# Performance work log

Hardware: AMD Instinct MI355X
Metric: run time of the kernel (lower is better)

## Reference

```python
import jax, jax.numpy as jnp
import numpy as np

C_IN = 256
C_RED = max(4, C_IN // 4)  # 64


def setup_inputs() -> dict:
    key = jax.random.key(0)
    k1, k2, k3, k4, k5 = jax.random.split(key, 5)
    B, C, H, W = 4, C_IN, 64, 64
    x = jax.random.normal(k1, (B, C, H, W), dtype=jnp.float32)
    # 1x1 convs (no bias) are just channel matmuls: weight shape (out_ch, in_ch)
    s_in = 1.0 / np.sqrt(C)
    s_red = 1.0 / np.sqrt(C_RED)
    Wq = jax.random.normal(k2, (C_RED, C), dtype=jnp.float32) * s_in
    Wk = jax.random.normal(k3, (C_RED, C), dtype=jnp.float32) * s_in
    Wv = jax.random.normal(k4, (C_RED, C), dtype=jnp.float32) * s_in
    Wp = jax.random.normal(k5, (C, C_RED), dtype=jnp.float32) * s_red
    return {"x": x, "Wq": Wq, "Wk": Wk, "Wv": Wv, "Wp": Wp}


def reference(x, Wq, Wk, Wv, Wp):
    B, C, H, W = x.shape
    N = H * W
    xf = x.reshape(B, C, N)                       # (B, C, N)
    q = jnp.einsum('rc,bcn->bnr', Wq, xf)         # (B, N, c_red)
    k = jnp.einsum('rc,bcn->brn', Wk, xf)         # (B, c_red, N)
    v = jnp.einsum('rc,bcn->bnr', Wv, xf)         # (B, N, c_red)
    scale = 1.0 / jnp.sqrt(jnp.float32(k.shape[1]))
    attn = jnp.einsum('bnr,brm->bnm', q, k) * scale   # (B, N, N)
    attn = jax.nn.softmax(attn, axis=-1)
    out = jnp.einsum('bnm,bmr->brn', attn, v)     # (B, c_red, N)
    out = jnp.einsum('cr,brn->bcn', Wp, out)      # (B, C, N)
    return out.reshape(B, C, H, W) + x
```

## Files before the change

### kernel.cpp

```cpp
#include <hip/hip_runtime.h>
#include <hip/hip_bf16.h>

#define CIN 256
#define CRED 64
#define NB 4
#define NN 4096

typedef float v4f __attribute__((ext_vector_type(4)));
typedef short v8s __attribute__((ext_vector_type(8)));
typedef unsigned short u16;
typedef u16 u16x4 __attribute__((ext_vector_type(4)));
typedef u16 u16x8 __attribute__((ext_vector_type(8)));
typedef unsigned int u32;

#define LOG2E 1.4426950408889634f

__device__ __forceinline__ u16 f2bf(float f) {
    union { float f; u32 u; } v; v.f = f;
    u32 r = (v.u + 0x7FFFu + ((v.u >> 16) & 1u)) >> 16;
    return (u16)r;
}
__device__ __forceinline__ float bf2f(u16 s) {
    union { u32 u; float f; } v; v.u = ((u32)s) << 16;
    return v.f;
}
__device__ __forceinline__ v4f mfma16(v8s a, v8s b, v4f c) {
    return __builtin_amdgcn_mfma_f32_16x16x32_bf16(a, b, c, 0, 0, 0);
}
__device__ __forceinline__ float fexp2(float x) {
#if __has_builtin(__builtin_amdgcn_exp2f)
    return __builtin_amdgcn_exp2f(x);
#else
    return exp2f(x);
#endif
}

__global__ __launch_bounds__(256) void k_wconv(const float* __restrict__ Wq,
                                               const float* __restrict__ Wk,
                                               const float* __restrict__ Wv,
                                               const float* __restrict__ Wp,
                                               u16* __restrict__ Wb,
                                               u16* __restrict__ WpB) {
    int t = threadIdx.x;
    if (blockIdx.x < 48) {
        int idx = (blockIdx.x * 256 + t) * 4;
        int row = idx >> 8;
        int mat = row >> 6, r = row & 63, col = idx & 255;
        const float* src = (mat == 0) ? Wq : (mat == 1) ? Wk : Wv;
        float4 v = *(const float4*)&src[r * 256 + col];
        float s = (mat == 0) ? (0.125f * LOG2E) : 1.0f;
        u16x4 o;
        o[0] = f2bf(v.x * s); o[1] = f2bf(v.y * s);
        o[2] = f2bf(v.z * s); o[3] = f2bf(v.w * s);
        *(u16x4*)&Wb[idx] = o;
    } else {
        int idx = ((blockIdx.x - 48) * 256 + t) * 4;
        float4 v = *(const float4*)&Wp[idx];
        u16x4 o;
        o[0] = f2bf(v.x); o[1] = f2bf(v.y);
        o[2] = f2bf(v.z); o[3] = f2bf(v.w);
        *(u16x4*)&WpB[idx] = o;
    }
}

#define XP 264
__global__ __launch_bounds__(256, 2) void k_qkvm(const float* __restrict__ x,
                                                 const u16* __restrict__ Wb,
                                                 u16* __restrict__ Q, u16* __restrict__ K,
                                                 u16* __restrict__ V) {
    __shared__ u16 xT[32 * XP];
    __shared__ u16 Vt[4][16 * 20];
    int t = threadIdx.x;
    int wv = t >> 6, lane = t & 63, c15 = lane & 15, quad = lane >> 4;
    int n0g = blockIdx.x * 32;
    int b = n0g >> 12;
    int nb = n0g & 4095;
    const float* xb = x + ((size_t)b << 20) + nb;

#pragma unroll
    for (int i = 0; i < 8; ++i) {
        int f4 = t + i * 256;
        int c = f4 >> 3, j4 = (f4 & 7) * 4;
        float4 v = *(const float4*)&xb[(size_t)c * 4096 + j4];
        xT[(j4 + 0) * XP + c] = f2bf(v.x);
        xT[(j4 + 1) * XP + c] = f2bf(v.y);
        xT[(j4 + 2) * XP + c] = f2bf(v.z);
        xT[(j4 + 3) * XP + c] = f2bf(v.w);
    }
    __syncthreads();

#pragma unroll
    for (int rti = 0; rti < 3; ++rti) {
        int rt = wv * 3 + rti;
        const u16* wrow = Wb + (size_t)(rt * 16 + c15) * 256 + quad * 8;
        v8s Bf[8];
#pragma unroll
        for (int kc = 0; kc < 8; ++kc) Bf[kc] = *(const v8s*)&wrow[kc * 32];
#pragma unroll
        for (int nt = 0; nt < 2; ++nt) {
            v4f acc = {0.f, 0.f, 0.f, 0.f};
            const u16* arow = &xT[(nt * 16 + c15) * XP + quad * 8];
#pragma unroll
            for (int kc = 0; kc < 8; ++kc) {
                v8s Af = *(const v8s*)&arow[kc * 32];
                acc = mfma16(Af, Bf[kc], acc);
            }
            if (rt < 8) {
                u16* base = (rt < 4) ? Q : K;
                u16* dst = base + ((size_t)b << 18)
                         + (size_t)(nb + nt * 16 + quad * 4) * 64
                         + (rt & 3) * 16 + c15;
#pragma unroll
                for (int g = 0; g < 4; ++g) dst[g * 64] = f2bf(acc[g]);
            } else {
                u16* vt = Vt[wv];
#pragma unroll
                for (int g = 0; g < 4; ++g)
                    vt[c15 * 20 + quad * 4 + g] = f2bf(acc[g]);
                int r_loc = lane & 15, ng2 = lane >> 4;
                u16x4 vvv = *(u16x4*)&vt[r_loc * 20 + ng2 * 4];
                size_t va = ((size_t)b * 64 + (rt - 8) * 16 + r_loc) * 4096
                          + nb + nt * 16 + ng2 * 4;
                *(u16x4*)&V[va] = vvv;
            }
        }
    }
}

__global__ __launch_bounds__(256, 4) void k_flash(const u16* __restrict__ Q,
                                                  const u16* __restrict__ K,
                                                  const u16* __restrict__ V,
                                                  u16* __restrict__ OP,
                                                  float* __restrict__ Lb,
                                                  int sh) {
    __shared__ u16 Kl[64][72];
    __shared__ u16 Vl[64][72];
    __shared__ u16 Pl[4][32][72];
    int t = threadIdx.x;
    int p = blockIdx.x & ((1u << sh) - 1);
    int tile = blockIdx.x >> sh;
    int b = tile >> 5;
    int n0 = (tile & 31) * 128;
    int wv = t >> 6;
    int lane = t & 63;
    int c15 = lane & 15;
    int quad = lane >> 4;
    int nw = n0 + wv * 32;
    const u16* Qb = Q + (size_t)b * NN * 64;
    const u16* Kb = K + (size_t)b * NN * 64;
    const u16* Vb = V + (size_t)b * 64 * NN;

    v8s Qa[2][2];
#pragma unroll
    for (int rg = 0; rg < 2; ++rg)
#pragma unroll
        for (int c2 = 0; c2 < 2; ++c2)
            Qa[rg][c2] = *(const v8s*)&Qb[(size_t)(nw + rg * 16 + c15) * 64 + c2 * 32 + quad * 8];

    v4f O[2][4];
    float ls[2][4];
#pragma unroll
    for (int rg = 0; rg < 2; ++rg)
#pragma unroll
        for (int g = 0; g < 4; ++g) {
            ls[rg][g] = 0.f;
#pragma unroll
            for (int cg = 0; cg < 4; ++cg) O[rg][cg][g] = 0.f;
        }

    int mlen = NN >> sh;
    int m0 = p * mlen;
    int iters = mlen >> 6;
    for (int it = 0; it < iters; ++it) {
        int mt = m0 + it * 64;
        int srow = t >> 3, scol = (t & 7) * 8;
#pragma unroll
        for (int pass = 0; pass < 2; ++pass) {
            int rr = srow + pass * 32;
            *(v8s*)&Kl[rr][scol] = *(const v8s*)&Kb[(size_t)(mt + rr) * 64 + scol];
            *(v8s*)&Vl[rr][scol] = *(const v8s*)&Vb[(size_t)rr * NN + mt + scol];
        }
        __syncthreads();

        v4f S[2][4];
#pragma unroll
        for (int rg = 0; rg < 2; ++rg)
#pragma unroll
            for (int s = 0; s < 4; ++s)
#pragma unroll
                for (int g = 0; g < 4; ++g) S[rg][s][g] = 0.f;
#pragma unroll
        for (int s = 0; s < 4; ++s)
#pragma unroll
            for (int c2 = 0; c2 < 2; ++c2) {
                v8s kb = *(const v8s*)&Kl[s * 16 + c15][c2 * 32 + quad * 8];
                S[0][s] = mfma16(Qa[0][c2], kb, S[0][s]);
                S[1][s] = mfma16(Qa[1][c2], kb, S[1][s]);
            }

#pragma unroll
        for (int rg = 0; rg < 2; ++rg)
#pragma unroll
            for (int s = 0; s < 4; ++s)
#pragma unroll
                for (int g = 0; g < 4; ++g) {
                    float e = fexp2(S[rg][s][g]);
                    ls[rg][g] += e;
                    Pl[wv][rg * 16 + quad * 4 + g][s * 16 + c15] = f2bf(e);
                }

        v8s Pa[2][2];
#pragma unroll
        for (int rg = 0; rg < 2; ++rg)
#pragma unroll
            for (int c2 = 0; c2 < 2; ++c2)
                Pa[rg][c2] = *(const v8s*)&Pl[wv][rg * 16 + c15][c2 * 32 + quad * 8];
#pragma unroll
        for (int cg = 0; cg < 4; ++cg)
#pragma unroll
            for (int c2 = 0; c2 < 2; ++c2) {
                v8s vb = *(const v8s*)&Vl[cg * 16 + c15][c2 * 32 + quad * 8];
                O[0][cg] = mfma16(Pa[0][c2], vb, O[0][cg]);
                O[1][cg] = mfma16(Pa[1][c2], vb, O[1][cg]);
            }
        __syncthreads();
    }

    u16* OPp = OP + (size_t)p * (NB * NN * 64) + (size_t)b * NN * 64;
#pragma unroll
    for (int rg = 0; rg < 2; ++rg)
#pragma unroll
        for (int cg = 0; cg < 4; ++cg)
#pragma unroll
            for (int g = 0; g < 4; ++g) {
                int n = nw + rg * 16 + quad * 4 + g;
                OPp[(size_t)n * 64 + cg * 16 + c15] = f2bf(O[rg][cg][g]);
            }
#pragma unroll
    for (int rg = 0; rg < 2; ++rg)
#pragma unroll
        for (int g = 0; g < 4; ++g) {
            float v = ls[rg][g];
#pragma unroll
            for (int off = 1; off <= 8; off <<= 1) v += __shfl_xor(v, off);
            ls[rg][g] = v;
        }
    if (c15 == 0) {
        float* Lp = Lb + (size_t)p * (NB * NN) + (size_t)b * NN;
#pragma unroll
        for (int rg = 0; rg < 2; ++rg)
#pragma unroll
            for (int g = 0; g < 4; ++g) {
                int n = nw + rg * 16 + quad * 4 + g;
                Lp[n] = ls[rg][g];
            }
    }
}

#define OMP 72
__global__ __launch_bounds__(256) void k_proj(const u16* __restrict__ OP,
                                              const float* __restrict__ Lb,
                                              const u16* __restrict__ WpB,
                                              const float* __restrict__ x,
                                              float* __restrict__ out,
                                              int nsp) {
    __shared__ u16 Om[32 * OMP];
    int t = threadIdx.x;
    int b = blockIdx.x >> 7;
    int n0 = (blockIdx.x & 127) * 32;

    {
        int n_l = t >> 3, r0 = (t & 7) * 8;
        size_t nidx = (size_t)b * NN + n0 + n_l;
        float o[8];
#pragma unroll
        for (int j = 0; j < 8; ++j) o[j] = 0.f;
        float l = 0.f;
        for (int p = 0; p < nsp; ++p) {
            u16x8 u = *(const u16x8*)&OP[((size_t)p * (NB * NN) + nidx) * 64 + r0];
#pragma unroll
            for (int j = 0; j < 8; ++j) o[j] += bf2f(u[j]);
            l += Lb[(size_t)p * (NB * NN) + nidx];
        }
        float inv = 1.0f / l;
        u16x8 pk;
#pragma unroll
        for (int j = 0; j < 8; ++j) pk[j] = f2bf(o[j] * inv);
        *(u16x8*)&Om[n_l * OMP + r0] = pk;
    }
    __syncthreads();

    int lane = t & 63, wv = t >> 6, c15 = lane & 15, quad = lane >> 4;
#pragma unroll
    for (int ct0 = 0; ct0 < 4; ++ct0) {
        int ct = wv * 4 + ct0;
        const u16* wrow = WpB + (size_t)(ct * 16 + c15) * 64 + quad * 8;
        v8s A0 = *(const v8s*)&wrow[0];
        v8s A1 = *(const v8s*)&wrow[32];
#pragma unroll
        for (int nt = 0; nt < 2; ++nt) {
            v8s B0 = *(const v8s*)&Om[(nt * 16 + c15) * OMP + quad * 8];
            v8s B1 = *(const v8s*)&Om[(nt * 16 + c15) * OMP + 32 + quad * 8];
            v4f acc = {0.f, 0.f, 0.f, 0.f};
            acc = mfma16(A0, B0, acc);
            acc = mfma16(A1, B1, acc);
            int cb = ct * 16 + quad * 4;
            size_t base = ((size_t)b * 256 + cb) * 4096 + n0 + nt * 16 + c15;
#pragma unroll
            for (int g = 0; g < 4; ++g)
                out[base + (size_t)g * 4096] = acc[g] + x[base + (size_t)g * 4096];
        }
    }
}

extern "C" void kernel_launch(void* const* d_in, const int* in_sizes, int n_in,
                              void* d_out, int out_size, void* d_ws, size_t ws_size,
                              hipStream_t stream) {
    const float* x  = (const float*)d_in[0];
    const float* Wq = (const float*)d_in[1];
    const float* Wk = (const float*)d_in[2];
    const float* Wv = (const float*)d_in[3];
    const float* Wp = (const float*)d_in[4];
    float* out = (float*)d_out;
    char* ws = (char*)d_ws;

    int nsp = (ws_size >= (size_t)24 * 1024 * 1024) ? 8 : 4;
    int sh = (nsp == 8) ? 3 : 2;

    u16* Wb  = (u16*)(ws);
    u16* WpB = (u16*)(ws + 131072);
    u16* Q   = (u16*)(ws + 262144);
    u16* K   = (u16*)(ws + 262144 + 2097152);
    u16* V   = (u16*)(ws + 262144 + 2 * 2097152);
    u16* OP  = (u16*)(ws + 262144 + 3 * 2097152);
    float* Lbuf = (float*)(ws + 262144 + (size_t)(3 + nsp) * 2097152);

    k_wconv<<<64, 256, 0, stream>>>(Wq, Wk, Wv, Wp, Wb, WpB);
    k_qkvm<<<512, 256, 0, stream>>>(x, Wb, Q, K, V);
    k_flash<<<NB * 32 * nsp, 256, 0, stream>>>(Q, K, V, OP, Lbuf, sh);
    k_proj<<<512, 256, 0, stream>>>(OP, Lbuf, WpB, x, out, nsp);
}
```

Before: 127.1 us.

## Load x fragments straight to registers, permute V layout, pack P stores, shrink proj tiles

The QKV projection kernel now builds MFMA A fragments directly from global x with strided scalar loads and packed bf16 conversion, dropping the LDS transpose and its barrier. V is written in a permuted column order so that the flash kernel can store P with packed 4-element writes instead of scalar LDS stores. The flash kernel's P layout changes to match, and the projection kernel uses 16-column tiles with twice as many blocks. Strided uncoalesced global loads of x and scattered V stores may cost more bandwidth than the LDS work they replace.

```diff
diff --git a/kernel.cpp b/kernel.cpp
--- a/kernel.cpp
+++ b/kernel.cpp
@@ -23,6 +23,12 @@
 __device__ __forceinline__ float bf2f(u16 s) {
     union { u32 u; float f; } v; v.u = ((u32)s) << 16;
     return v.f;
+}
+__device__ __forceinline__ u32 pkbf(float a, float b) {
+    float2 f; f.x = a; f.y = b;
+    __hip_bfloat162 h = __float22bfloat162_rn(f);
+    union { __hip_bfloat162 h; u32 u; } c; c.h = h;
+    return c.u;
 }
 __device__ __forceinline__ v4f mfma16(v8s a, v8s b, v4f c) {
     return __builtin_amdgcn_mfma_f32_16x16x32_bf16(a, b, c, 0, 0, 0);
@@ -63,31 +69,32 @@
     }
 }
 
-#define XP 264
-__global__ __launch_bounds__(256, 2) void k_qkvm(const float* __restrict__ x,
-                                                 const u16* __restrict__ Wb,
-                                                 u16* __restrict__ Q, u16* __restrict__ K,
-                                                 u16* __restrict__ V) {
-    __shared__ u16 xT[32 * XP];
-    __shared__ u16 Vt[4][16 * 20];
+__global__ __launch_bounds__(256) void k_qkvm(const float* __restrict__ x,
+                                              const u16* __restrict__ Wb,
+                                              u16* __restrict__ Q, u16* __restrict__ K,
+                                              u16* __restrict__ V) {
     int t = threadIdx.x;
     int wv = t >> 6, lane = t & 63, c15 = lane & 15, quad = lane >> 4;
     int n0g = blockIdx.x * 32;
-    int b = n0g >> 12;
-    int nb = n0g & 4095;
-    const float* xb = x + ((size_t)b << 20) + nb;
-
-#pragma unroll
-    for (int i = 0; i < 8; ++i) {
-        int f4 = t + i * 256;
-        int c = f4 >> 3, j4 = (f4 & 7) * 4;
-        float4 v = *(const float4*)&xb[(size_t)c * 4096 + j4];
-        xT[(j4 + 0) * XP + c] = f2bf(v.x);
-        xT[(j4 + 1) * XP + c] = f2bf(v.y);
-        xT[(j4 + 2) * XP + c] = f2bf(v.z);
-        xT[(j4 + 3) * XP + c] = f2bf(v.w);
-    }
-    __syncthreads();
+    int b = n0g >> 12, nb = n0g & 4095;
+    const float* xb = x + ((size_t)b << 20);
+
+    v8s Af[2][8];
+#pragma unroll
+    for (int nt = 0; nt < 2; ++nt) {
+        const float* px = xb + nb + nt * 16 + c15 + (size_t)quad * 8 * 4096;
+#pragma unroll
+        for (int kc = 0; kc < 8; ++kc) {
+            float f[8];
+#pragma unroll
+            for (int j = 0; j < 8; ++j)
+                f[j] = px[((size_t)kc * 32 + j) * 4096];
+            union { v8s s; u32 w[4]; } pk;
+            pk.w[0] = pkbf(f[0], f[1]); pk.w[1] = pkbf(f[2], f[3]);
+            pk.w[2] = pkbf(f[4], f[5]); pk.w[3] = pkbf(f[6], f[7]);
+            Af[nt][kc] = pk.s;
+        }
+    }
 
 #pragma unroll
     for (int rti = 0; rti < 3; ++rti) {
@@ -99,12 +106,9 @@
 #pragma unroll
         for (int nt = 0; nt < 2; ++nt) {
             v4f acc = {0.f, 0.f, 0.f, 0.f};
-            const u16* arow = &xT[(nt * 16 + c15) * XP + quad * 8];
-#pragma unroll
-            for (int kc = 0; kc < 8; ++kc) {
-                v8s Af = *(const v8s*)&arow[kc * 32];
-                acc = mfma16(Af, Bf[kc], acc);
-            }
+#pragma unroll
+            for (int kc = 0; kc < 8; ++kc)
+                acc = mfma16(Af[nt][kc], Bf[kc], acc);
             if (rt < 8) {
                 u16* base = (rt < 4) ? Q : K;
                 u16* dst = base + ((size_t)b << 18)
@@ -113,15 +117,12 @@
 #pragma unroll
                 for (int g = 0; g < 4; ++g) dst[g * 64] = f2bf(acc[g]);
             } else {
-                u16* vt = Vt[wv];
+                int hi2 = ((nb + nt * 16) >> 4) & 3;
+                size_t base = ((size_t)b * 64 + (rt - 8) * 16 + c15) * 4096
+                            + (size_t)((nb + nt * 16) & ~63) + hi2;
 #pragma unroll
                 for (int g = 0; g < 4; ++g)
-                    vt[c15 * 20 + quad * 4 + g] = f2bf(acc[g]);
-                int r_loc = lane & 15, ng2 = lane >> 4;
-                u16x4 vvv = *(u16x4*)&vt[r_loc * 20 + ng2 * 4];
-                size_t va = ((size_t)b * 64 + (rt - 8) * 16 + r_loc) * 4096
-                          + nb + nt * 16 + ng2 * 4;
-                *(u16x4*)&V[va] = vvv;
+                    V[base + (quad * 4 + g) * 4] = f2bf(acc[g]);
             }
         }
     }
@@ -199,15 +200,24 @@
             }
 
 #pragma unroll
-        for (int rg = 0; rg < 2; ++rg)
+        for (int rg = 0; rg < 2; ++rg) {
+            float E[4][4];
 #pragma unroll
             for (int s = 0; s < 4; ++s)
 #pragma unroll
                 for (int g = 0; g < 4; ++g) {
                     float e = fexp2(S[rg][s][g]);
+                    E[s][g] = e;
                     ls[rg][g] += e;
-                    Pl[wv][rg * 16 + quad * 4 + g][s * 16 + c15] = f2bf(e);
                 }
+#pragma unroll
+            for (int g = 0; g < 4; ++g) {
+                union { u16x4 v; u32 w[2]; } p2;
+                p2.w[0] = pkbf(E[0][g], E[1][g]);
+                p2.w[1] = pkbf(E[2][g], E[3][g]);
+                *(u16x4*)&Pl[wv][rg * 16 + quad * 4 + g][c15 * 4] = p2.v;
+            }
+        }
 
         v8s Pa[2][2];
 #pragma unroll
@@ -264,52 +274,46 @@
                                               const float* __restrict__ x,
                                               float* __restrict__ out,
                                               int nsp) {
-    __shared__ u16 Om[32 * OMP];
+    __shared__ u16 Om[16 * OMP];
     int t = threadIdx.x;
-    int b = blockIdx.x >> 7;
-    int n0 = (blockIdx.x & 127) * 32;
+    int b = blockIdx.x >> 8;
+    int n0 = (blockIdx.x & 255) * 16;
 
     {
-        int n_l = t >> 3, r0 = (t & 7) * 8;
+        int n_l = t >> 4, r0 = (t & 15) * 4;
         size_t nidx = (size_t)b * NN + n0 + n_l;
-        float o[8];
-#pragma unroll
-        for (int j = 0; j < 8; ++j) o[j] = 0.f;
+        float o[4] = {0.f, 0.f, 0.f, 0.f};
         float l = 0.f;
         for (int p = 0; p < nsp; ++p) {
-            u16x8 u = *(const u16x8*)&OP[((size_t)p * (NB * NN) + nidx) * 64 + r0];
-#pragma unroll
-            for (int j = 0; j < 8; ++j) o[j] += bf2f(u[j]);
+            u16x4 u = *(const u16x4*)&OP[((size_t)p * (NB * NN) + nidx) * 64 + r0];
+#pragma unroll
+            for (int j = 0; j < 4; ++j) o[j] += bf2f(u[j]);
             l += Lb[(size_t)p * (NB * NN) + nidx];
         }
         float inv = 1.0f / l;
-        u16x8 pk;
-#pragma unroll
-        for (int j = 0; j < 8; ++j) pk[j] = f2bf(o[j] * inv);
-        *(u16x8*)&Om[n_l * OMP + r0] = pk;
+        union { u16x4 v; u32 w[2]; } p2;
+        p2.w[0] = pkbf(o[0] * inv, o[1] * inv);
+        p2.w[1] = pkbf(o[2] * inv, o[3] * inv);
+        *(u16x4*)&Om[n_l * OMP + r0] = p2.v;
     }
     __syncthreads();
 
-    int lane = t & 63, wv = t >> 6, c15 = lane & 15, quad = lane >> 4;
+    int lane = t & 63, wvv = t >> 6, c15 = lane & 15, quad = lane >> 4;
+    v8s B0 = *(const v8s*)&Om[c15 * OMP + quad * 8];
+    v8s B1 = *(const v8s*)&Om[c15 * OMP + 32 + quad * 8];
 #pragma unroll
     for (int ct0 = 0; ct0 < 4; ++ct0) {
-        int ct = wv * 4 + ct0;
+        int ct = wvv * 4 + ct0;
         const u16* wrow = WpB + (size_t)(ct * 16 + c15) * 64 + quad * 8;
         v8s A0 = *(const v8s*)&wrow[0];
         v8s A1 = *(const v8s*)&wrow[32];
-#pragma unroll
-        for (int nt = 0; nt < 2; ++nt) {
-            v8s B0 = *(const v8s*)&Om[(nt * 16 + c15) * OMP + quad * 8];
-            v8s B1 = *(const v8s*)&Om[(nt * 16 + c15) * OMP + 32 + quad * 8];
-            v4f acc = {0.f, 0.f, 0.f, 0.f};
-            acc = mfma16(A0, B0, acc);
-            acc = mfma16(A1, B1, acc);
-            int cb = ct * 16 + quad * 4;
-            size_t base = ((size_t)b * 256 + cb) * 4096 + n0 + nt * 16 + c15;
-#pragma unroll
-            for (int g = 0; g < 4; ++g)
-                out[base + (size_t)g * 4096] = acc[g] + x[base + (size_t)g * 4096];
-        }
+        v4f acc = {0.f, 0.f, 0.f, 0.f};
+        acc = mfma16(A0, B0, acc);
+        acc = mfma16(A1, B1, acc);
+        size_t base = ((size_t)(b * 256 + ct * 16 + quad * 4)) * 4096 + n0 + c15;
+#pragma unroll
+        for (int g = 0; g < 4; ++g)
+            out[base + (size_t)g * 4096] = acc[g] + x[base + (size_t)g * 4096];
     }
 }
 
@@ -338,5 +342,5 @@
     k_wconv<<<64, 256, 0, stream>>>(Wq, Wk, Wv, Wp, Wb, WpB);
     k_qkvm<<<512, 256, 0, stream>>>(x, Wb, Q, K, V);
     k_flash<<<NB * 32 * nsp, 256, 0, stream>>>(Q, K, V, OP, Lbuf, sh);
-    k_proj<<<512, 256, 0, stream>>>(OP, Lbuf, WpB, x, out, nsp);
-}
+    k_proj<<<NB * 256, 256, 0, stream>>>(OP, Lbuf, WpB, x, out, nsp);
+}
```

New measurement: 126.5 us. About the same (-0.5%).
